# Performance work log

Measured on AMD Instinct MI355X. Metric: run time of the kernel, lower is better.

Reference implementation:

```python
import jax, jax.numpy as jnp
import numpy as np

B, S, D, H = 2, 2048, 1024, 16
DK = D // H


def setup_inputs() -> dict:
    key = jax.random.key(0)
    ks = jax.random.split(key, 11)
    scale = 1.0 / np.sqrt(D)
    inp = {
        "q": jax.random.normal(ks[0], (B, S, D), jnp.float32),
        "k": jax.random.normal(ks[1], (B, S, D), jnp.float32),
        "v": jax.random.normal(ks[2], (B, S, D), jnp.float32),
        # causal mask, broadcastable to (B, H, S, S); 0 = masked
        "mask": jnp.tril(jnp.ones((S, S), jnp.int32))[None, None, :, :],
        "wq": jax.random.normal(ks[3], (D, D), jnp.float32) * scale,
        "bq": jax.random.normal(ks[4], (D,), jnp.float32) * scale,
        "wk": jax.random.normal(ks[5], (D, D), jnp.float32) * scale,
        "bk": jax.random.normal(ks[6], (D,), jnp.float32) * scale,
        "wv": jax.random.normal(ks[7], (D, D), jnp.float32) * scale,
        "bv": jax.random.normal(ks[8], (D,), jnp.float32) * scale,
        "wo": jax.random.normal(ks[9], (D, D), jnp.float32) * scale,
        "bo": jax.random.normal(ks[10], (D,), jnp.float32) * scale,
    }
    return inp


def reference(q, k, v, mask, wq, bq, wk, bk, wv, bv, wo, bo):
    # Linear projections (torch Linear: y = x @ W^T + b)
    Q = jnp.einsum('bsd,ed->bse', q, wq) + bq
    K = jnp.einsum('bsd,ed->bse', k, wk) + bk
    V = jnp.einsum('bsd,ed->bse', v, wv) + bv
    # split heads -> (B, H, S, d_k)
    Q = Q.reshape(B, S, H, DK).transpose(0, 2, 1, 3)
    K = K.reshape(B, S, H, DK).transpose(0, 2, 1, 3)
    V = V.reshape(B, S, H, DK).transpose(0, 2, 1, 3)
    # naive full-score attention, faithful to the source
    scores = jnp.einsum('bhqd,bhkd->bhqk', Q, K) / jnp.sqrt(jnp.float32(DK))
    scores = jnp.where(mask == 0, -jnp.inf, scores)
    attn = jax.nn.softmax(scores, axis=-1)
    out = jnp.einsum('bhqk,bhkd->bhqd', attn, V)
    # merge heads -> (B, S, D)
    out = out.transpose(0, 2, 1, 3).reshape(B, S, D)
    return jnp.einsum('bsd,ed->bse', out, wo) + bo
```

## Files before the change

### kernel.cpp

```cpp
#include <hip/hip_runtime.h>
#include <hip/hip_bf16.h>
#include <cstdint>

constexpr int Bc = 2, Sc = 2048, Dc = 1024, Hc = 16;
constexpr int Mtok = Bc * Sc;

typedef __bf16 bf16;
typedef __bf16 bf16x4 __attribute__((ext_vector_type(4)));
typedef __bf16 bf16x8 __attribute__((ext_vector_type(8)));
typedef float  f32x4  __attribute__((ext_vector_type(4)));

__device__ __forceinline__ void gld_lds16(const bf16* g, bf16* l) {
  __builtin_amdgcn_global_load_lds(
      (__attribute__((address_space(1))) void*)(void*)g,
      (__attribute__((address_space(3))) void*)l, 16, 0, 0);
}

__global__ __launch_bounds__(256) void convert_all(
    const float* __restrict__ q, const float* __restrict__ k,
    const float* __restrict__ v, const float* __restrict__ wq,
    const float* __restrict__ wk, const float* __restrict__ wv,
    const float* __restrict__ wo, bf16* __restrict__ ws)
{
  constexpr size_t NQ = (size_t)Mtok * Dc;
  constexpr size_t NW = (size_t)Dc * Dc;
  const size_t e = ((size_t)blockIdx.x * 256 + threadIdx.x) * 8;
  const float* src; bf16* dst;
  if (e < 3 * NQ) {
    src = (e < NQ) ? q + e : (e < 2 * NQ) ? k + (e - NQ) : v + (e - 2 * NQ);
    dst = ws + e;
  } else {
    const size_t w = e - 3 * NQ;
    const float* wsrc = (w < NW) ? wq : (w < 2 * NW) ? wk : (w < 3 * NW) ? wv : wo;
    src = wsrc + (w & (NW - 1));
    dst = ws + 5 * NQ + w;
  }
  f32x4 a = ((const f32x4*)src)[0];
  f32x4 b = ((const f32x4*)src)[1];
  bf16x8 t;
  t[0]=(bf16)a[0]; t[1]=(bf16)a[1]; t[2]=(bf16)a[2]; t[3]=(bf16)a[3];
  t[4]=(bf16)b[0]; t[5]=(bf16)b[1]; t[6]=(bf16)b[2]; t[7]=(bf16)b[3];
  *(bf16x8*)dst = t;
}

__global__ __launch_bounds__(256) void gemm_qkv(
    const bf16* __restrict__ Aq, const bf16* __restrict__ Ak,
    const bf16* __restrict__ Av, const bf16* __restrict__ Wb,
    const float* __restrict__ bq, const float* __restrict__ bk,
    const float* __restrict__ bv,
    bf16* __restrict__ Yq, bf16* __restrict__ Yk, bf16* __restrict__ Vt)
{
  __shared__ __attribute__((aligned(16))) bf16 As[128 * 64];
  __shared__ __attribute__((aligned(16))) bf16 Bs[128 * 64];

  const int z = blockIdx.z;
  const bf16*  A    = (z == 0) ? Aq : (z == 1) ? Ak : Av;
  const bf16*  Wz   = Wb + (size_t)z * Dc * Dc;
  const float* bias = (z == 0) ? bq : (z == 1) ? bk : bv;

  const int m0 = blockIdx.x * 128, n0 = blockIdx.y * 128;
  const int tid = threadIdx.x, wave = tid >> 6, lane = tid & 63;
  const int quad = lane >> 4, l16 = lane & 15;
  const int rw = wave >> 1, cw = wave & 1;
  const int swz = l16 & 7;
  const int srow = wave * 8 + (lane >> 3);
  const int scol = ((lane & 7) ^ (lane >> 3)) * 8;

  f32x4 acc[4][4] = {};

  for (int k0 = 0; k0 < Dc; k0 += 64) {
#pragma unroll
    for (int s = 0; s < 4; ++s) {
      gld_lds16(A  + (size_t)(m0 + s * 32 + srow) * Dc + k0 + scol,
                &As[(s * 32 + wave * 8) * 64]);
      gld_lds16(Wz + (size_t)(n0 + s * 32 + srow) * Dc + k0 + scol,
                &Bs[(s * 32 + wave * 8) * 64]);
    }
    __syncthreads();
#pragma unroll
    for (int ks = 0; ks < 2; ++ks) {
      bf16x8 af[4];
#pragma unroll
      for (int rt = 0; rt < 4; ++rt)
        af[rt] = *(const bf16x8*)
            &As[(rw * 64 + rt * 16 + l16) * 64 + (((ks * 4 + quad) ^ swz) * 8)];
#pragma unroll
      for (int ct = 0; ct < 4; ++ct) {
        bf16x8 bfr = *(const bf16x8*)
            &Bs[(cw * 64 + ct * 16 + l16) * 64 + (((ks * 4 + quad) ^ swz) * 8)];
#pragma unroll
        for (int rt = 0; rt < 4; ++rt)
          acc[rt][ct] = __builtin_amdgcn_mfma_f32_16x16x32_bf16(af[rt], bfr, acc[rt][ct], 0, 0, 0);
      }
    }
    __syncthreads();
  }

  if (z < 2) {
    bf16* Y = (z == 0) ? Yq : Yk;
#pragma unroll
    for (int ct = 0; ct < 4; ++ct) {
      const int col = n0 + cw * 64 + ct * 16 + l16;
      const float bvv = bias[col];
#pragma unroll
      for (int rt = 0; rt < 4; ++rt)
#pragma unroll
        for (int i = 0; i < 4; ++i) {
          const int row = m0 + rw * 64 + rt * 16 + quad * 4 + i;
          Y[(size_t)row * Dc + col] = (bf16)(acc[rt][ct][i] + bvv);
        }
    }
  } else {
#pragma unroll
    for (int ct = 0; ct < 4; ++ct) {
      const int col = n0 + cw * 64 + ct * 16 + l16;
      const float bvv = bias[col];
#pragma unroll
      for (int rt = 0; rt < 4; ++rt) {
        const int row0 = m0 + rw * 64 + rt * 16 + quad * 4;
        const int bb = row0 >> 11, s0 = row0 & 2047;
        bf16x4 pk;
#pragma unroll
        for (int i = 0; i < 4; ++i) pk[i] = (bf16)(acc[rt][ct][i] + bvv);
        *(bf16x4*)&Vt[((size_t)bb * Dc + col) * Sc + s0] = pk;
      }
    }
  }
}

__global__ __launch_bounds__(256) void gemm_o(
    const bf16* __restrict__ A, const bf16* __restrict__ Wz,
    const float* __restrict__ bias, float* __restrict__ Y)
{
  __shared__ __attribute__((aligned(16))) bf16 As[64 * 64];
  __shared__ __attribute__((aligned(16))) bf16 Bs[128 * 64];

  const int m0 = blockIdx.x * 64, n0 = blockIdx.y * 128;
  const int tid = threadIdx.x, wave = tid >> 6, lane = tid & 63;
  const int quad = lane >> 4, l16 = lane & 15;
  const int swz = l16 & 7;
  const int srow = wave * 8 + (lane >> 3);
  const int scol = ((lane & 7) ^ (lane >> 3)) * 8;

  f32x4 acc[4][2] = {};

  for (int k0 = 0; k0 < Dc; k0 += 64) {
#pragma unroll
    for (int s = 0; s < 2; ++s)
      gld_lds16(A + (size_t)(m0 + s * 32 + srow) * Dc + k0 + scol,
                &As[(s * 32 + wave * 8) * 64]);
#pragma unroll
    for (int s = 0; s < 4; ++s)
      gld_lds16(Wz + (size_t)(n0 + s * 32 + srow) * Dc + k0 + scol,
                &Bs[(s * 32 + wave * 8) * 64]);
    __syncthreads();
#pragma unroll
    for (int ks = 0; ks < 2; ++ks) {
      bf16x8 af[4];
#pragma unroll
      for (int rt = 0; rt < 4; ++rt)
        af[rt] = *(const bf16x8*)
            &As[(rt * 16 + l16) * 64 + (((ks * 4 + quad) ^ swz) * 8)];
#pragma unroll
      for (int ct = 0; ct < 2; ++ct) {
        bf16x8 bfr = *(const bf16x8*)
            &Bs[(wave * 32 + ct * 16 + l16) * 64 + (((ks * 4 + quad) ^ swz) * 8)];
#pragma unroll
        for (int rt = 0; rt < 4; ++rt)
          acc[rt][ct] = __builtin_amdgcn_mfma_f32_16x16x32_bf16(af[rt], bfr, acc[rt][ct], 0, 0, 0);
      }
    }
    __syncthreads();
  }

#pragma unroll
  for (int ct = 0; ct < 2; ++ct) {
    const int col = n0 + wave * 32 + ct * 16 + l16;
    const float bvv = bias[col];
#pragma unroll
    for (int rt = 0; rt < 4; ++rt)
#pragma unroll
      for (int i = 0; i < 4; ++i) {
        const int row = m0 + rt * 16 + quad * 4 + i;
        Y[(size_t)row * Dc + col] = acc[rt][ct][i] + bvv;
      }
  }
}

template <bool AF32, bool BF32, bool OUTF32>
__global__ __launch_bounds__(256) void gemm128(
    const void* __restrict__ Av, const void* __restrict__ Bv,
    const float* __restrict__ bias, void* __restrict__ Yv,
    int M, int N, int K)
{
  __shared__ __attribute__((aligned(16))) bf16 As[2][128][40];
  __shared__ __attribute__((aligned(16))) bf16 Bs[2][128][40];

  const int m0 = blockIdx.x * 128, n0 = blockIdx.y * 128;
  const int tid = threadIdx.x, wave = tid >> 6, lane = tid & 63;
  const int quad = lane >> 4, l16 = lane & 15;
  const int rw = wave >> 1, cw = wave & 1;
  const int srow = tid >> 1, sc = (tid & 1) * 16;

  f32x4 acc[4][4] = {};

  auto load = [&](const void* P, bool f32, int r0, int k0, bf16x8& lo, bf16x8& hi) {
    if (f32) {
      const float* s = (const float*)P + (size_t)(r0 + srow) * K + k0 + sc;
      f32x4 a0 = ((const f32x4*)s)[0], a1 = ((const f32x4*)s)[1];
      f32x4 a2 = ((const f32x4*)s)[2], a3 = ((const f32x4*)s)[3];
      lo[0]=(bf16)a0[0]; lo[1]=(bf16)a0[1]; lo[2]=(bf16)a0[2]; lo[3]=(bf16)a0[3];
      lo[4]=(bf16)a1[0]; lo[5]=(bf16)a1[1]; lo[6]=(bf16)a1[2]; lo[7]=(bf16)a1[3];
      hi[0]=(bf16)a2[0]; hi[1]=(bf16)a2[1]; hi[2]=(bf16)a2[2]; hi[3]=(bf16)a2[3];
      hi[4]=(bf16)a3[0]; hi[5]=(bf16)a3[1]; hi[6]=(bf16)a3[2]; hi[7]=(bf16)a3[3];
    } else {
      const bf16* s = (const bf16*)P + (size_t)(r0 + srow) * K + k0 + sc;
      lo = ((const bf16x8*)s)[0]; hi = ((const bf16x8*)s)[1];
    }
  };

  bf16x8 alo, ahi, blo, bhi;
  load(Av, AF32, m0, 0, alo, ahi); load(Bv, BF32, n0, 0, blo, bhi);
  *(bf16x8*)&As[0][srow][sc] = alo; *(bf16x8*)&As[0][srow][sc + 8] = ahi;
  *(bf16x8*)&Bs[0][srow][sc] = blo; *(bf16x8*)&Bs[0][srow][sc + 8] = bhi;

  const int NIT = K >> 5;
  for (int it = 0; it < NIT; ++it) {
    __syncthreads();
    const int cur = it & 1;
    const bool pf = (it + 1) < NIT;
    if (pf) { load(Av, AF32, m0, (it+1)*32, alo, ahi); load(Bv, BF32, n0, (it+1)*32, blo, bhi); }

    bf16x8 af[4];
#pragma unroll
    for (int rt = 0; rt < 4; ++rt)
      af[rt] = *(const bf16x8*)&As[cur][rw * 64 + rt * 16 + l16][quad * 8];
#pragma unroll
    for (int ct = 0; ct < 4; ++ct) {
      bf16x8 bfr = *(const bf16x8*)&Bs[cur][cw * 64 + ct * 16 + l16][quad * 8];
#pragma unroll
      for (int rt = 0; rt < 4; ++rt)
        acc[rt][ct] = __builtin_amdgcn_mfma_f32_16x16x32_bf16(af[rt], bfr, acc[rt][ct], 0, 0, 0);
    }
    if (pf) {
      const int nxt = cur ^ 1;
      *(bf16x8*)&As[nxt][srow][sc] = alo; *(bf16x8*)&As[nxt][srow][sc + 8] = ahi;
      *(bf16x8*)&Bs[nxt][srow][sc] = blo; *(bf16x8*)&Bs[nxt][srow][sc + 8] = bhi;
    }
  }

#pragma unroll
  for (int ct = 0; ct < 4; ++ct) {
    const int col = n0 + cw * 64 + ct * 16 + l16;
    const float bvv = bias[col];
#pragma unroll
    for (int rt = 0; rt < 4; ++rt)
#pragma unroll
      for (int i = 0; i < 4; ++i) {
        const int row = m0 + rw * 64 + rt * 16 + quad * 4 + i;
        const float vv = acc[rt][ct][i] + bvv;
        if constexpr (OUTF32) ((float*)Yv)[(size_t)row * N + col] = vv;
        else                  ((bf16*)Yv)[(size_t)row * N + col] = (bf16)vv;
      }
  }
}

__global__ __launch_bounds__(256) void transpose_v(
    const bf16* __restrict__ in, bf16* __restrict__ out)
{
  __shared__ __attribute__((aligned(16))) bf16 tile[64][72];
  const int s0 = blockIdx.x * 64, d0 = blockIdx.y * 64, b = blockIdx.z;
  const int t = threadIdx.x, r = t >> 2, c = (t & 3) * 16;

  const bf16* src = in + (size_t)(b * Sc + s0 + r) * Dc + d0 + c;
  *(bf16x8*)&tile[r][c]     = ((const bf16x8*)src)[0];
  *(bf16x8*)&tile[r][c + 8] = ((const bf16x8*)src)[1];
  __syncthreads();

  bf16x8 t0, t1;
#pragma unroll
  for (int j = 0; j < 8; ++j) t0[j] = tile[c + j][r];
#pragma unroll
  for (int j = 0; j < 8; ++j) t1[j] = tile[c + 8 + j][r];
  bf16* dst = out + (size_t)(b * Dc + d0 + r) * Sc + s0 + c;
  ((bf16x8*)dst)[0] = t0;
  ((bf16x8*)dst)[1] = t1;
}

__global__ __launch_bounds__(256) void attn4(
    const bf16* __restrict__ Q, const bf16* __restrict__ K,
    const bf16* __restrict__ Vt, bf16* __restrict__ O)
{
  __shared__ __attribute__((aligned(16))) bf16 Ks[2][64][68];
  __shared__ __attribute__((aligned(16))) bf16 Vs[2][64][68];
  __shared__ __attribute__((aligned(16))) bf16 Ps[4][16][68];

  const int bh = blockIdx.x, b = bh >> 4, h = bh & 15;
  const int qy = blockIdx.y;
  const int qt = (qy & 8) ? ((qy & 24) | (7 - (qy & 7))) : qy;
  const int q0 = qt * 64;
  const int nkb = qt + 1;

  const int tid = threadIdx.x, wave = tid >> 6, lane = tid & 63;
  const int quad = lane >> 4, l16 = lane & 15;
  const int sr = tid >> 2, sc4 = (tid & 3) * 16;

  const bf16 onec = (bf16)1.0f;
  const bf16x8 ones = {onec, onec, onec, onec, onec, onec, onec, onec};

  const bf16* qrow = Q + (size_t)(b * Sc + q0 + wave * 16 + l16) * Dc + h * 64 + quad * 8;
  const bf16x8 aq0 = *(const bf16x8*)qrow;
  const bf16x8 aq1 = *(const bf16x8*)(qrow + 32);

  f32x4 oacc[4] = {{0,0,0,0},{0,0,0,0},{0,0,0,0},{0,0,0,0}};
  f32x4 lacc = {0, 0, 0, 0};

  {
    const bf16* ksrc = K + (size_t)(b * Sc + sr) * Dc + h * 64 + sc4;
    ((bf16x8*)&Ks[0][sr][sc4])[0] = ((const bf16x8*)ksrc)[0];
    ((bf16x8*)&Ks[0][sr][sc4])[1] = ((const bf16x8*)ksrc)[1];
    const bf16* vsrc = Vt + (size_t)(b * Dc + h * 64 + sr) * Sc + sc4;
    ((bf16x8*)&Vs[0][sr][sc4])[0] = ((const bf16x8*)vsrc)[0];
    ((bf16x8*)&Vs[0][sr][sc4])[1] = ((const bf16x8*)vsrc)[1];
  }

  for (int kb = 0; kb < nkb; ++kb) {
    __syncthreads();
    const int cur = kb & 1;
    const bool pf = (kb + 1) < nkb;
    bf16x8 kp0, kp1, vp0, vp1;
    if (pf) {
      const bf16* ksrc = K + (size_t)(b * Sc + (kb + 1) * 64 + sr) * Dc + h * 64 + sc4;
      kp0 = ((const bf16x8*)ksrc)[0]; kp1 = ((const bf16x8*)ksrc)[1];
      const bf16* vsrc = Vt + (size_t)(b * Dc + h * 64 + sr) * Sc + (kb + 1) * 64 + sc4;
      vp0 = ((const bf16x8*)vsrc)[0]; vp1 = ((const bf16x8*)vsrc)[1];
    }

    f32x4 s[4] = {{0,0,0,0},{0,0,0,0},{0,0,0,0},{0,0,0,0}};
#pragma unroll
    for (int d2 = 0; d2 < 2; ++d2) {
      const bf16x8 bq = d2 ? aq1 : aq0;
#pragma unroll
      for (int ct = 0; ct < 4; ++ct) {
        bf16x8 ak = *(const bf16x8*)&Ks[cur][ct * 16 + l16][d2 * 32 + quad * 8];
        s[ct] = __builtin_amdgcn_mfma_f32_16x16x32_bf16(ak, bq, s[ct], 0, 0, 0);
      }
    }

    if (kb == nkb - 1) {
      const int qcol = wave * 16 + l16;
#pragma unroll
      for (int ct = 0; ct < 4; ++ct) {
        const int key0 = ct * 16 + quad * 4;
        bf16x4 pk;
#pragma unroll
        for (int i = 0; i < 4; ++i)
          pk[i] = (bf16)((key0 + i > qcol) ? 0.f : __expf(s[ct][i] * 0.125f));
        *(bf16x4*)&Ps[wave][l16][key0] = pk;
      }
    } else {
#pragma unroll
      for (int ct = 0; ct < 4; ++ct) {
        bf16x4 pk;
#pragma unroll
        for (int i = 0; i < 4; ++i) pk[i] = (bf16)__expf(s[ct][i] * 0.125f);
        *(bf16x4*)&Ps[wave][l16][ct * 16 + quad * 4] = pk;
      }
    }

    const bf16x8 ap0 = *(const bf16x8*)&Ps[wave][l16][quad * 8];
    const bf16x8 ap1 = *(const bf16x8*)&Ps[wave][l16][32 + quad * 8];

    lacc = __builtin_amdgcn_mfma_f32_16x16x32_bf16(ap0, ones, lacc, 0, 0, 0);
    lacc = __builtin_amdgcn_mfma_f32_16x16x32_bf16(ap1, ones, lacc, 0, 0, 0);

#pragma unroll
    for (int d2 = 0; d2 < 2; ++d2) {
      const bf16x8 ap = d2 ? ap1 : ap0;
#pragma unroll
      for (int ct = 0; ct < 4; ++ct) {
        bf16x8 bv = *(const bf16x8*)&Vs[cur][ct * 16 + l16][d2 * 32 + quad * 8];
        oacc[ct] = __builtin_amdgcn_mfma_f32_16x16x32_bf16(ap, bv, oacc[ct], 0, 0, 0);
      }
    }

    if (pf) {
      const int nxt = cur ^ 1;
      ((bf16x8*)&Ks[nxt][sr][sc4])[0] = kp0; ((bf16x8*)&Ks[nxt][sr][sc4])[1] = kp1;
      ((bf16x8*)&Vs[nxt][sr][sc4])[0] = vp0; ((bf16x8*)&Vs[nxt][sr][sc4])[1] = vp1;
    }
  }

  f32x4 rl;
#pragma unroll
  for (int i = 0; i < 4; ++i) rl[i] = 1.0f / lacc[i];
#pragma unroll
  for (int ct = 0; ct < 4; ++ct)
#pragma unroll
    for (int i = 0; i < 4; ++i)
      O[(size_t)(b * Sc + q0 + wave * 16 + quad * 4 + i) * Dc + h * 64 + ct * 16 + l16] =
          (bf16)(oacc[ct][i] * rl[i]);
}

extern "C" void kernel_launch(void* const* d_in, const int* in_sizes, int n_in,
                              void* d_out, int out_size, void* d_ws, size_t ws_size,
                              hipStream_t stream)
{
  const float* q  = (const float*)d_in[0];
  const float* k  = (const float*)d_in[1];
  const float* v  = (const float*)d_in[2];
  const float* wq = (const float*)d_in[4];
  const float* bq = (const float*)d_in[5];
  const float* wk = (const float*)d_in[6];
  const float* bk = (const float*)d_in[7];
  const float* wv = (const float*)d_in[8];
  const float* bv = (const float*)d_in[9];
  const float* wo = (const float*)d_in[10];
  const float* bo = (const float*)d_in[11];
  float* out = (float*)d_out;

  constexpr size_t NQ = (size_t)Mtok * Dc;
  constexpr size_t NW = (size_t)Dc * Dc;
  bf16* W = (bf16*)d_ws;
  const dim3 ga(Hc * Bc, 32);
  const dim3 gt(Sc / 64, Dc / 64, Bc);

  const bool fancy = ws_size >= (size_t)(6 * NQ + 4 * NW) * 2;
  if (fancy) {
    bf16* xq = W;
    bf16* xk = W + NQ;
    bf16* xv = W + 2 * NQ;
    bf16* Qp = W + 3 * NQ;
    bf16* Kp = W + 4 * NQ;
    bf16* wb = W + 5 * NQ;
    bf16* Vt = W + 5 * NQ + 4 * NW;
    bf16* AO = W;

    convert_all<<<8192, 256, 0, stream>>>(q, k, v, wq, wk, wv, wo, W);
    gemm_qkv<<<dim3(Mtok / 128, Dc / 128, 3), 256, 0, stream>>>(
        xq, xk, xv, wb, bq, bk, bv, Qp, Kp, Vt);
    attn4<<<ga, 256, 0, stream>>>(Qp, Kp, Vt, AO);
    gemm_o<<<dim3(Mtok / 64, Dc / 128), 256, 0, stream>>>(AO, wb + 3 * NW, bo, out);
  } else {
    bf16* Qp = W;
    bf16* Kp = W + NQ;
    bf16* Vp = W + 2 * NQ;
    bf16* Vt = W + 3 * NQ;
    bf16* AO = W + 4 * NQ;
    const dim3 gg(Mtok / 128, Dc / 128);
    gemm128<true, true, false><<<gg, 256, 0, stream>>>(q, wq, bq, Qp, Mtok, Dc, Dc);
    gemm128<true, true, false><<<gg, 256, 0, stream>>>(k, wk, bk, Kp, Mtok, Dc, Dc);
    gemm128<true, true, false><<<gg, 256, 0, stream>>>(v, wv, bv, Vp, Mtok, Dc, Dc);
    transpose_v<<<gt, 256, 0, stream>>>(Vp, Vt);
    attn4<<<ga, 256, 0, stream>>>(Qp, Kp, Vt, AO);
    gemm128<false, true, true><<<gg, 256, 0, stream>>>(AO, wo, bo, out, Mtok, Dc, Dc);
  }
}
```

Before: 228.1 us.

## Use direct global-to-LDS loads in attention and enlarge output GEMM tile to 128x128

The attention kernel drops its register-staged double-buffered K/V prefetch. It now loads each K/V tile straight into a swizzled single-buffered LDS layout using global_load_lds, with an extra barrier per block, and adds an occupancy hint in launch_bounds. The output projection GEMM moves from 64x128 to 128x128 tiles, with a 2x2 wave layout where each wave owns a 64x64 subtile, so operand reuse goes up and the grid gets smaller. The trade-off is less load/compute overlap in attention, since the prefetch is gone, and fewer blocks for the output GEMM.

```diff
diff --git a/kernel.cpp b/kernel.cpp
--- a/kernel.cpp
+++ b/kernel.cpp
@@ -132,27 +132,27 @@
     const bf16* __restrict__ A, const bf16* __restrict__ Wz,
     const float* __restrict__ bias, float* __restrict__ Y)
 {
-  __shared__ __attribute__((aligned(16))) bf16 As[64 * 64];
+  __shared__ __attribute__((aligned(16))) bf16 As[128 * 64];
   __shared__ __attribute__((aligned(16))) bf16 Bs[128 * 64];
 
-  const int m0 = blockIdx.x * 64, n0 = blockIdx.y * 128;
+  const int m0 = blockIdx.x * 128, n0 = blockIdx.y * 128;
   const int tid = threadIdx.x, wave = tid >> 6, lane = tid & 63;
   const int quad = lane >> 4, l16 = lane & 15;
+  const int rw = wave >> 1, cw = wave & 1;
   const int swz = l16 & 7;
   const int srow = wave * 8 + (lane >> 3);
   const int scol = ((lane & 7) ^ (lane >> 3)) * 8;
 
-  f32x4 acc[4][2] = {};
+  f32x4 acc[4][4] = {};
 
   for (int k0 = 0; k0 < Dc; k0 += 64) {
 #pragma unroll
-    for (int s = 0; s < 2; ++s)
-      gld_lds16(A + (size_t)(m0 + s * 32 + srow) * Dc + k0 + scol,
+    for (int s = 0; s < 4; ++s) {
+      gld_lds16(A  + (size_t)(m0 + s * 32 + srow) * Dc + k0 + scol,
                 &As[(s * 32 + wave * 8) * 64]);
-#pragma unroll
-    for (int s = 0; s < 4; ++s)
       gld_lds16(Wz + (size_t)(n0 + s * 32 + srow) * Dc + k0 + scol,
                 &Bs[(s * 32 + wave * 8) * 64]);
+    }
     __syncthreads();
 #pragma unroll
     for (int ks = 0; ks < 2; ++ks) {
@@ -160,11 +160,11 @@
 #pragma unroll
       for (int rt = 0; rt < 4; ++rt)
         af[rt] = *(const bf16x8*)
-            &As[(rt * 16 + l16) * 64 + (((ks * 4 + quad) ^ swz) * 8)];
-#pragma unroll
-      for (int ct = 0; ct < 2; ++ct) {
+            &As[(rw * 64 + rt * 16 + l16) * 64 + (((ks * 4 + quad) ^ swz) * 8)];
+#pragma unroll
+      for (int ct = 0; ct < 4; ++ct) {
         bf16x8 bfr = *(const bf16x8*)
-            &Bs[(wave * 32 + ct * 16 + l16) * 64 + (((ks * 4 + quad) ^ swz) * 8)];
+            &Bs[(cw * 64 + ct * 16 + l16) * 64 + (((ks * 4 + quad) ^ swz) * 8)];
 #pragma unroll
         for (int rt = 0; rt < 4; ++rt)
           acc[rt][ct] = __builtin_amdgcn_mfma_f32_16x16x32_bf16(af[rt], bfr, acc[rt][ct], 0, 0, 0);
@@ -174,14 +174,14 @@
   }
 
 #pragma unroll
-  for (int ct = 0; ct < 2; ++ct) {
-    const int col = n0 + wave * 32 + ct * 16 + l16;
+  for (int ct = 0; ct < 4; ++ct) {
+    const int col = n0 + cw * 64 + ct * 16 + l16;
     const float bvv = bias[col];
 #pragma unroll
     for (int rt = 0; rt < 4; ++rt)
 #pragma unroll
       for (int i = 0; i < 4; ++i) {
-        const int row = m0 + rt * 16 + quad * 4 + i;
+        const int row = m0 + rw * 64 + rt * 16 + quad * 4 + i;
         Y[(size_t)row * Dc + col] = acc[rt][ct][i] + bvv;
       }
   }
@@ -287,12 +287,12 @@
   ((bf16x8*)dst)[1] = t1;
 }
 
-__global__ __launch_bounds__(256) void attn4(
+__global__ __launch_bounds__(256, 6) void attn5(
     const bf16* __restrict__ Q, const bf16* __restrict__ K,
     const bf16* __restrict__ Vt, bf16* __restrict__ O)
 {
-  __shared__ __attribute__((aligned(16))) bf16 Ks[2][64][68];
-  __shared__ __attribute__((aligned(16))) bf16 Vs[2][64][68];
+  __shared__ __attribute__((aligned(16))) bf16 Ks[64 * 64];
+  __shared__ __attribute__((aligned(16))) bf16 Vs[64 * 64];
   __shared__ __attribute__((aligned(16))) bf16 Ps[4][16][68];
 
   const int bh = blockIdx.x, b = bh >> 4, h = bh & 15;
@@ -303,7 +303,9 @@
 
   const int tid = threadIdx.x, wave = tid >> 6, lane = tid & 63;
   const int quad = lane >> 4, l16 = lane & 15;
-  const int sr = tid >> 2, sc4 = (tid & 3) * 16;
+  const int swz = l16 & 7;
+  const int sr  = lane >> 3;
+  const int sgc = ((lane & 7) ^ sr) * 8;
 
   const bf16 onec = (bf16)1.0f;
   const bf16x8 ones = {onec, onec, onec, onec, onec, onec, onec, onec};
@@ -315,26 +317,17 @@
   f32x4 oacc[4] = {{0,0,0,0},{0,0,0,0},{0,0,0,0},{0,0,0,0}};
   f32x4 lacc = {0, 0, 0, 0};
 
-  {
-    const bf16* ksrc = K + (size_t)(b * Sc + sr) * Dc + h * 64 + sc4;
-    ((bf16x8*)&Ks[0][sr][sc4])[0] = ((const bf16x8*)ksrc)[0];
-    ((bf16x8*)&Ks[0][sr][sc4])[1] = ((const bf16x8*)ksrc)[1];
-    const bf16* vsrc = Vt + (size_t)(b * Dc + h * 64 + sr) * Sc + sc4;
-    ((bf16x8*)&Vs[0][sr][sc4])[0] = ((const bf16x8*)vsrc)[0];
-    ((bf16x8*)&Vs[0][sr][sc4])[1] = ((const bf16x8*)vsrc)[1];
-  }
-
   for (int kb = 0; kb < nkb; ++kb) {
     __syncthreads();
-    const int cur = kb & 1;
-    const bool pf = (kb + 1) < nkb;
-    bf16x8 kp0, kp1, vp0, vp1;
-    if (pf) {
-      const bf16* ksrc = K + (size_t)(b * Sc + (kb + 1) * 64 + sr) * Dc + h * 64 + sc4;
-      kp0 = ((const bf16x8*)ksrc)[0]; kp1 = ((const bf16x8*)ksrc)[1];
-      const bf16* vsrc = Vt + (size_t)(b * Dc + h * 64 + sr) * Sc + (kb + 1) * 64 + sc4;
-      vp0 = ((const bf16x8*)vsrc)[0]; vp1 = ((const bf16x8*)vsrc)[1];
-    }
+#pragma unroll
+    for (int j = 0; j < 2; ++j) {
+      const int r = wave * 16 + j * 8 + sr;
+      gld_lds16(K  + (size_t)(b * Sc + kb * 64 + r) * Dc + h * 64 + sgc,
+                &Ks[(wave * 16 + j * 8) * 64]);
+      gld_lds16(Vt + (size_t)(b * Dc + h * 64 + r) * Sc + kb * 64 + sgc,
+                &Vs[(wave * 16 + j * 8) * 64]);
+    }
+    __syncthreads();
 
     f32x4 s[4] = {{0,0,0,0},{0,0,0,0},{0,0,0,0},{0,0,0,0}};
 #pragma unroll
@@ -342,7 +335,8 @@
       const bf16x8 bq = d2 ? aq1 : aq0;
 #pragma unroll
       for (int ct = 0; ct < 4; ++ct) {
-        bf16x8 ak = *(const bf16x8*)&Ks[cur][ct * 16 + l16][d2 * 32 + quad * 8];
+        bf16x8 ak = *(const bf16x8*)
+            &Ks[(ct * 16 + l16) * 64 + (((d2 * 4 + quad) ^ swz) * 8)];
         s[ct] = __builtin_amdgcn_mfma_f32_16x16x32_bf16(ak, bq, s[ct], 0, 0, 0);
       }
     }
@@ -379,15 +373,10 @@
       const bf16x8 ap = d2 ? ap1 : ap0;
 #pragma unroll
       for (int ct = 0; ct < 4; ++ct) {
-        bf16x8 bv = *(const bf16x8*)&Vs[cur][ct * 16 + l16][d2 * 32 + quad * 8];
+        bf16x8 bv = *(const bf16x8*)
+            &Vs[(ct * 16 + l16) * 64 + (((d2 * 4 + quad) ^ swz) * 8)];
         oacc[ct] = __builtin_amdgcn_mfma_f32_16x16x32_bf16(ap, bv, oacc[ct], 0, 0, 0);
       }
-    }
-
-    if (pf) {
-      const int nxt = cur ^ 1;
-      ((bf16x8*)&Ks[nxt][sr][sc4])[0] = kp0; ((bf16x8*)&Ks[nxt][sr][sc4])[1] = kp1;
-      ((bf16x8*)&Vs[nxt][sr][sc4])[0] = vp0; ((bf16x8*)&Vs[nxt][sr][sc4])[1] = vp1;
     }
   }
 
@@ -439,8 +428,8 @@
     convert_all<<<8192, 256, 0, stream>>>(q, k, v, wq, wk, wv, wo, W);
     gemm_qkv<<<dim3(Mtok / 128, Dc / 128, 3), 256, 0, stream>>>(
         xq, xk, xv, wb, bq, bk, bv, Qp, Kp, Vt);
-    attn4<<<ga, 256, 0, stream>>>(Qp, Kp, Vt, AO);
-    gemm_o<<<dim3(Mtok / 64, Dc / 128), 256, 0, stream>>>(AO, wb + 3 * NW, bo, out);
+    attn5<<<ga, 256, 0, stream>>>(Qp, Kp, Vt, AO);
+    gemm_o<<<dim3(Mtok / 128, Dc / 128), 256, 0, stream>>>(AO, wb + 3 * NW, bo, out);
   } else {
     bf16* Qp = W;
     bf16* Kp = W + NQ;
@@ -452,7 +441,7 @@
     gemm128<true, true, false><<<gg, 256, 0, stream>>>(k, wk, bk, Kp, Mtok, Dc, Dc);
     gemm128<true, true, false><<<gg, 256, 0, stream>>>(v, wv, bv, Vp, Mtok, Dc, Dc);
     transpose_v<<<gt, 256, 0, stream>>>(Vp, Vt);
-    attn4<<<ga, 256, 0, stream>>>(Qp, Kp, Vt, AO);
+    attn5<<<ga, 256, 0, stream>>>(Qp, Kp, Vt, AO);
     gemm128<false, true, true><<<gg, 256, 0, stream>>>(AO, wo, bo, out, Mtok, Dc, Dc);
   }
 }
```

Measured after the change: 228.5 us. About the same (+0.2%).
